# Kernel tuning notes

Hardware: AMD Instinct MI355X
Metric: run time of the kernel (lower is better)

Reference implementation:

```python
import jax, jax.numpy as jnp
import numpy as np

N, E, DIM, HEADS, EDGE_DIM = 50000, 800000, 128, 4, 1
C = DIM // HEADS  # per-head channels
EPS = 1e-5


def graph_ln(h, w, b):
    # PyG LayerNorm, mode='graph', batch=None: normalize over ALL nodes+features
    mu = h.mean()
    hc = h - mu
    std = jnp.sqrt(jnp.mean(hc * hc))
    return hc / (std + EPS) * w + b


def setup_inputs() -> dict:
    key = jax.random.key(0)
    ks = jax.random.split(key, 16)
    s = 1.0 / np.sqrt(DIM)
    return {
        "x": jax.random.normal(ks[0], (N, DIM), jnp.float32),
        "edge_index": jax.random.randint(ks[1], (2, E), 0, N, jnp.int32),
        "edge_weight": jax.random.uniform(ks[2], (E,), jnp.float32),
        "edge_attr": jax.random.normal(ks[3], (E, EDGE_DIM), jnp.float32),
        # GCNConv params
        "W_gcn": jax.random.normal(ks[4], (DIM, DIM), jnp.float32) * s,
        "b_gcn": jnp.zeros((DIM,), jnp.float32),
        # GATv2Conv params (share_weights=True -> single lin)
        "W_l": jax.random.normal(ks[5], (DIM, DIM), jnp.float32) * s,
        "b_l": jnp.zeros((DIM,), jnp.float32),
        "W_edge": jax.random.normal(ks[6], (EDGE_DIM, DIM), jnp.float32),
        "att": jax.random.normal(ks[7], (HEADS, C), jnp.float32) * (1.0 / np.sqrt(C)),
        "b_gat": jnp.zeros((DIM,), jnp.float32),
        # norms
        "gcn_nw": jnp.ones((DIM,), jnp.float32), "gcn_nb": jnp.zeros((DIM,), jnp.float32),
        "gat_nw": jnp.ones((DIM,), jnp.float32), "gat_nb": jnp.zeros((DIM,), jnp.float32),
        "out_nw": jnp.ones((DIM,), jnp.float32), "out_nb": jnp.zeros((DIM,), jnp.float32),
        "alpha": jnp.ones((2,), jnp.float32),
    }


def reference(x, edge_index, edge_weight, edge_attr, W_gcn, b_gcn, W_l, b_l,
              W_edge, att, b_gat, gcn_nw, gcn_nb, gat_nw, gat_nb, out_nw, out_nb, alpha):
    src, dst = edge_index[0], edge_index[1]

    # ---- GCN branch (normalize=True, add_self_loops=False) ----
    deg = jax.ops.segment_sum(edge_weight, dst, num_segments=N)
    dis = jnp.where(deg > 0, jax.lax.rsqrt(jnp.maximum(deg, 1e-30)), 0.0)
    norm = dis[src] * edge_weight * dis[dst]  # [E]
    xw = x @ W_gcn  # [N, DIM]
    h = jax.ops.segment_sum(norm[:, None] * xw[src], dst, num_segments=N) + b_gcn
    gcn_out = x + jax.nn.gelu(graph_ln(h, gcn_nw, gcn_nb), approximate=False)

    # ---- GATv2 branch (share_weights=True, edge_dim=1) ----
    xl = (x @ W_l + b_l).reshape(N, HEADS, C)
    e = (edge_attr @ W_edge).reshape(E, HEADS, C)
    z = jax.nn.leaky_relu(xl[dst] + xl[src] + e, negative_slope=0.2)  # [E,H,C]
    logits = jnp.einsum('ehc,hc->eh', z, att)  # [E,H]
    m = jax.ops.segment_max(logits, dst, num_segments=N)  # [N,H]
    a = jnp.exp(logits - m[dst])
    denom = jax.ops.segment_sum(a, dst, num_segments=N)
    a = a / (denom[dst] + 1e-16)  # softmax over incoming edges per dst, per head
    msg = xl[src] * a[:, :, None]  # [E,H,C]
    g = jax.ops.segment_sum(msg, dst, num_segments=N).reshape(N, DIM) + b_gat
    gat_out = x + jax.nn.gelu(graph_ln(g, gat_nw, gat_nb), approximate=False)

    # ---- fuse ----
    w = jax.nn.softmax(alpha)
    fused = w[0] * gcn_out + w[1] * gat_out
    return jax.nn.gelu(graph_ln(fused, out_nw, out_nb), approximate=False)
```

## Files before the change

### kernel.cpp

```cpp
#include <hip/hip_runtime.h>
#include <math.h>

#define DIM 128
#define HEADS 4
#define EPS 1e-5f
#define NBLK 1024

__device__ __forceinline__ float us2f(unsigned short u) {
  union { unsigned int i; float f; } c; c.i = ((unsigned int)u) << 16; return c.f;
}
__device__ __forceinline__ unsigned short f2us(float f) {
  union { float ff; unsigned int i; } c; c.ff = f;
  return (unsigned short)((c.i + 0x7FFFu + ((c.i >> 16) & 1u)) >> 16);
}
__device__ __forceinline__ float ldf(const void* p, size_t i, int fl32) {
  return fl32 ? ((const float*)p)[i] : us2f(((const unsigned short*)p)[i]);
}
__device__ __forceinline__ float gelu_exact(float v) {
  return 0.5f * v * (1.0f + erff(v * 0.7071067811865475f));
}

__device__ __forceinline__ int packed_pos(int c) { return ((c & ~1) << 1) | (c & 1); }

__global__ void __launch_bounds__(256)
k_detect(const unsigned short* __restrict__ x, long n, int* __restrict__ dflag) {
  long lim = n < 8192 ? n : 8192;
  int bad = 0;
  for (long i = threadIdx.x; i < lim; i += 256) {
    float v = us2f(x[i]);
    float a = fabsf(v);
    if (!(a == 0.0f || (a > 1e-30f && a < 1e3f))) bad++;
  }
  __shared__ int sb[256];
  sb[threadIdx.x] = bad;
  __syncthreads();
  for (int off = 128; off > 0; off >>= 1) {
    if ((int)threadIdx.x < off) sb[threadIdx.x] += sb[threadIdx.x + off];
    __syncthreads();
  }
  if (threadIdx.x == 0) dflag[0] = (sb[0] > 32) ? 1 : 0;
}

__global__ void k_deg_cnt(const int* __restrict__ dst, const void* __restrict__ ew,
                          float* __restrict__ deg, int* __restrict__ cnt,
                          int* __restrict__ rank, int E, const int* __restrict__ df) {
  const int fl32 = *df;
  int e = blockIdx.x * blockDim.x + threadIdx.x;
  if (e < E) {
    int d = dst[e];
    rank[e] = atomicAdd(&cnt[d], 1);
    float w = ldf(ew, e, fl32);
    if (isfinite(w)) atomicAdd(&deg[d], w);
  }
}

__global__ void k_dis(float* __restrict__ deg, int N) {
  int i = blockIdx.x * blockDim.x + threadIdx.x;
  if (i < N) {
    float d = deg[i];
    deg[i] = (d > 0.0f) ? rsqrtf(fmaxf(d, 1e-30f)) : 0.0f;
  }
}

__global__ void __launch_bounds__(256)
k_scan(const int* __restrict__ cnt, int* __restrict__ off, int N, int E) {
  __shared__ int part[256];
  int t = threadIdx.x;
  int chunk = (N + 255) / 256;
  int lo = t * chunk;
  int hi = lo + chunk; if (hi > N) hi = N;
  int s = 0;
  for (int i = lo; i < hi; ++i) s += cnt[i];
  part[t] = s;
  __syncthreads();
  if (t == 0) {
    int run = 0;
    for (int j = 0; j < 256; ++j) { int tmp = part[j]; part[j] = run; run += tmp; }
  }
  __syncthreads();
  int run = part[t];
  for (int i = lo; i < hi; ++i) { off[i] = run; run += cnt[i]; }
  if (t == 0) off[N] = E;
}

__global__ void k_scatter(const int* __restrict__ src, const int* __restrict__ dst,
                          const void* __restrict__ ew, const void* __restrict__ ea,
                          const float* __restrict__ dis, const int* __restrict__ off,
                          const int* __restrict__ rank, int4* __restrict__ csr,
                          int E, const int* __restrict__ df) {
  const int fl32 = *df;
  int e = blockIdx.x * blockDim.x + threadIdx.x;
  if (e >= E) return;
  int d = dst[e], s = src[e];
  int pos = off[d] + rank[e];
  float nm = dis[s] * ldf(ew, e, fl32) * dis[d];
  if (!isfinite(nm)) nm = 0.0f;
  float eav = ldf(ea, e, fl32);
  if (!isfinite(eav)) eav = 0.0f;
  csr[pos] = make_int4(s, __float_as_int(nm), __float_as_int(eav), 0);
}

__global__ void __launch_bounds__(128)
k_gemm(const void* __restrict__ x, const void* __restrict__ Wg,
       const void* __restrict__ Wl, const void* __restrict__ bl,
       unsigned short* __restrict__ packed, int N, const int* __restrict__ df) {
  const int fl32 = *df;
  const int R = 8;
  __shared__ float xs[R][DIM];
  int c = threadIdx.x;
  int r0 = blockIdx.x * R;
  for (int r = 0; r < R; ++r) {
    int row = r0 + r;
    xs[r][c] = (row < N) ? ldf(x, (size_t)row * DIM + c, fl32) : 0.0f;
  }
  __syncthreads();
  float accg[R], accl[R];
  float blc = ldf(bl, c, fl32);
  #pragma unroll
  for (int r = 0; r < R; ++r) { accg[r] = 0.0f; accl[r] = blc; }
  for (int k = 0; k < DIM; ++k) {
    float wg = ldf(Wg, k * DIM + c, fl32);
    float wl = ldf(Wl, k * DIM + c, fl32);
    #pragma unroll
    for (int r = 0; r < R; ++r) {
      accg[r] = fmaf(xs[r][k], wg, accg[r]);
      accl[r] = fmaf(xs[r][k], wl, accl[r]);
    }
  }
  int pos = packed_pos(c);
  for (int r = 0; r < R; ++r) {
    int row = r0 + r;
    if (row < N) {
      float ag = accg[r], al = accl[r];
      if (!isfinite(ag)) ag = 0.0f;
      if (!isfinite(al)) al = 0.0f;
      packed[(size_t)row * 256 + pos] = f2us(al);
      packed[(size_t)row * 256 + pos + 2] = f2us(ag);
    }
  }
}

__global__ void __launch_bounds__(256)
k_mega(const int* __restrict__ off, const int4* __restrict__ csr,
       const unsigned short* __restrict__ packed,
       const void* __restrict__ Wed, const void* __restrict__ att,
       const void* __restrict__ bgcn, const void* __restrict__ bgat,
       float* __restrict__ h, float* __restrict__ g,
       double* __restrict__ pA, double* __restrict__ pB, int N,
       const int* __restrict__ df) {
  const int fl32 = *df;
  int wid = threadIdx.x >> 6;
  int lane = threadIdx.x & 63;
  int node = blockIdx.x * 4 + wid;
  int c0 = lane * 2;
  float wd0 = ldf(Wed, c0, fl32), wd1 = ldf(Wed, c0 + 1, fl32);
  float at0 = ldf(att, c0, fl32), at1 = ldf(att, c0 + 1, fl32);
  double sA = 0.0, sA2 = 0.0, sB = 0.0, sB2 = 0.0;
  if (node < N) {
    int beg = off[node], end = off[node + 1];
    ushort4 xd = *(const ushort4*)(packed + (size_t)node * 256 + lane * 4);
    float xd0 = us2f(xd.x), xd1 = us2f(xd.y);
    float mx = -INFINITY, den = 0.f;
    float ga0 = 0.f, ga1 = 0.f, hc0 = 0.f, hc1 = 0.f;
    int4 cP = make_int4(0, 0, 0, 0);
    ushort4 vP = make_ushort4(0, 0, 0, 0);
    if (beg < end) {
      cP = csr[beg];
      vP = *(const ushort4*)(packed + (size_t)cP.x * 256 + lane * 4);
    }
    for (int i = beg; i < end; ++i) {
      int4 ce = cP; ushort4 v = vP;
      if (i + 1 < end) {
        cP = csr[i + 1];
        vP = *(const ushort4*)(packed + (size_t)cP.x * 256 + lane * 4);
      }
      float nm = __int_as_float(ce.y), eav = __int_as_float(ce.z);
      float vx = us2f(v.x), vy = us2f(v.y);
      float z0 = xd0 + vx + eav * wd0; z0 = (z0 > 0.f) ? z0 : 0.2f * z0;
      float z1 = xd1 + vy + eav * wd1; z1 = (z1 > 0.f) ? z1 : 0.2f * z1;
      float dot = z0 * at0 + z1 * at1;
      dot += __shfl_xor(dot, 1);
      dot += __shfl_xor(dot, 2);
      dot += __shfl_xor(dot, 4);
      dot += __shfl_xor(dot, 8);
      float e = __expf(-fabsf(dot - mx));
      bool up = dot > mx;
      float corr = up ? e : 1.0f;
      float w = up ? 1.0f : e;
      mx = up ? dot : mx;
      den = fmaf(den, corr, w);
      ga0 = fmaf(ga0, corr, w * vx);
      ga1 = fmaf(ga1, corr, w * vy);
      hc0 = fmaf(nm, us2f(v.z), hc0);
      hc1 = fmaf(nm, us2f(v.w), hc1);
    }
    float inv = (end > beg) ? 1.0f / (den + 1e-16f) : 0.0f;
    ga0 *= inv; ga1 *= inv;
    if (!isfinite(ga0)) ga0 = 0.0f;
    if (!isfinite(ga1)) ga1 = 0.0f;
    if (!isfinite(hc0)) hc0 = 0.0f;
    if (!isfinite(hc1)) hc1 = 0.0f;
    *(float2*)(h + (size_t)node * DIM + c0) = make_float2(hc0, hc1);
    *(float2*)(g + (size_t)node * DIM + c0) = make_float2(ga0, ga1);
    float hA0 = hc0 + ldf(bgcn, c0, fl32), hA1 = hc1 + ldf(bgcn, c0 + 1, fl32);
    float gB0 = ga0 + ldf(bgat, c0, fl32), gB1 = ga1 + ldf(bgat, c0 + 1, fl32);
    sA  = (double)hA0 + (double)hA1;
    sA2 = (double)hA0 * hA0 + (double)hA1 * hA1;
    sB  = (double)gB0 + (double)gB1;
    sB2 = (double)gB0 * gB0 + (double)gB1 * gB1;
  }
  __shared__ double l1[256], l2[256], l3[256], l4[256];
  l1[threadIdx.x] = sA; l2[threadIdx.x] = sA2; l3[threadIdx.x] = sB; l4[threadIdx.x] = sB2;
  __syncthreads();
  for (int o = 128; o > 0; o >>= 1) {
    if ((int)threadIdx.x < o) {
      l1[threadIdx.x] += l1[threadIdx.x + o];
      l2[threadIdx.x] += l2[threadIdx.x + o];
      l3[threadIdx.x] += l3[threadIdx.x + o];
      l4[threadIdx.x] += l4[threadIdx.x + o];
    }
    __syncthreads();
  }
  if (threadIdx.x == 0) {
    pA[2 * blockIdx.x] = l1[0]; pA[2 * blockIdx.x + 1] = l2[0];
    pB[2 * blockIdx.x] = l3[0]; pB[2 * blockIdx.x + 1] = l4[0];
  }
}

__device__ __forceinline__ void ln_params(double S, double S2, double M, float* mu_out, float* sc_out) {
  double mu = S / M;
  double v = S2 / M - mu * mu;
  if (!(v > 0.0)) v = 0.0;
  float fmu = (float)mu;
  float sc = 1.0f / ((float)sqrt(v) + EPS);
  if (!isfinite(fmu)) fmu = 0.0f;
  if (!isfinite(sc)) sc = 0.0f;
  *mu_out = fmu; *sc_out = sc;
}

__global__ void __launch_bounds__(256)
k_fin12(const double* __restrict__ pA, const double* __restrict__ pB, int nblk,
        const void* __restrict__ alpha, float* __restrict__ params, double M,
        const int* __restrict__ df) {
  const int fl32 = *df;
  __shared__ double l1[256], l2[256], l3[256], l4[256];
  double a = 0, b = 0, c = 0, d = 0;
  for (int j = threadIdx.x; j < nblk; j += 256) {
    a += pA[2 * j]; b += pA[2 * j + 1];
    c += pB[2 * j]; d += pB[2 * j + 1];
  }
  l1[threadIdx.x] = a; l2[threadIdx.x] = b; l3[threadIdx.x] = c; l4[threadIdx.x] = d;
  __syncthreads();
  for (int off = 128; off > 0; off >>= 1) {
    if ((int)threadIdx.x < off) {
      l1[threadIdx.x] += l1[threadIdx.x + off];
      l2[threadIdx.x] += l2[threadIdx.x + off];
      l3[threadIdx.x] += l3[threadIdx.x + off];
      l4[threadIdx.x] += l4[threadIdx.x + off];
    }
    __syncthreads();
  }
  if (threadIdx.x == 0) {
    ln_params(l1[0], l2[0], M, &params[0], &params[1]);
    ln_params(l3[0], l4[0], M, &params[2], &params[3]);
    float a0 = ldf(alpha, 0, fl32), a1 = ldf(alpha, 1, fl32);
    if (!isfinite(a0)) a0 = 0.0f;
    if (!isfinite(a1)) a1 = 0.0f;
    float mx = fmaxf(a0, a1);
    float e0 = expf(a0 - mx), e1 = expf(a1 - mx);
    float inv = 1.0f / (e0 + e1);
    params[4] = e0 * inv;
    params[5] = e1 * inv;
  }
}

__global__ void __launch_bounds__(256)
k_fin3(const double* __restrict__ pC, float* __restrict__ params, double M) {
  __shared__ double l1[256], l2[256];
  double a = 0, b = 0;
  for (int j = threadIdx.x; j < NBLK; j += 256) { a += pC[2 * j]; b += pC[2 * j + 1]; }
  l1[threadIdx.x] = a; l2[threadIdx.x] = b;
  __syncthreads();
  for (int off = 128; off > 0; off >>= 1) {
    if ((int)threadIdx.x < off) {
      l1[threadIdx.x] += l1[threadIdx.x + off];
      l2[threadIdx.x] += l2[threadIdx.x + off];
    }
    __syncthreads();
  }
  if (threadIdx.x == 0) ln_params(l1[0], l2[0], M, &params[6], &params[7]);
}

__global__ void __launch_bounds__(256)
k_fuse(const void* __restrict__ x, float* h, const float* __restrict__ g,
       const void* __restrict__ b_gcn, const void* __restrict__ b_gat,
       const void* __restrict__ gcn_nw, const void* __restrict__ gcn_nb,
       const void* __restrict__ gat_nw, const void* __restrict__ gat_nb,
       const float* __restrict__ params, double* __restrict__ pC, long n,
       const int* __restrict__ df) {
  const int fl32 = *df;
  float mu1 = params[0], sc1 = params[1], mu2 = params[2], sc2 = params[3];
  float w0 = params[4], w1 = params[5];
  double s = 0.0, s2 = 0.0;
  long stride = (long)gridDim.x * blockDim.x;
  for (long i = (long)blockIdx.x * blockDim.x + threadIdx.x; i < n; i += stride) {
    size_t c = (size_t)(i & (DIM - 1));
    float xv = ldf(x, i, fl32);
    float hv = h[i] + ldf(b_gcn, c, fl32);
    float gv = g[i] + ldf(b_gat, c, fl32);
    float go = xv + gelu_exact((hv - mu1) * sc1 * ldf(gcn_nw, c, fl32) + ldf(gcn_nb, c, fl32));
    float ao = xv + gelu_exact((gv - mu2) * sc2 * ldf(gat_nw, c, fl32) + ldf(gat_nb, c, fl32));
    float f = w0 * go + w1 * ao;
    if (!isfinite(f)) f = 0.0f;
    h[i] = f;
    s += f; s2 += (double)f * f;
  }
  __shared__ double ls[256], ls2[256];
  ls[threadIdx.x] = s; ls2[threadIdx.x] = s2;
  __syncthreads();
  for (int off = 128; off > 0; off >>= 1) {
    if ((int)threadIdx.x < off) {
      ls[threadIdx.x] += ls[threadIdx.x + off];
      ls2[threadIdx.x] += ls2[threadIdx.x + off];
    }
    __syncthreads();
  }
  if (threadIdx.x == 0) { pC[2 * blockIdx.x] = ls[0]; pC[2 * blockIdx.x + 1] = ls2[0]; }
}

__global__ void k_final(const float* __restrict__ fused, const void* __restrict__ nw,
                        const void* __restrict__ nb, const float* __restrict__ params,
                        void* __restrict__ out, long n, const int* __restrict__ df) {
  const int fl32 = *df;
  long i = (long)blockIdx.x * blockDim.x + threadIdx.x;
  if (i >= n) return;
  size_t c = (size_t)(i & (DIM - 1));
  float mu = params[6], sc = params[7];
  float r = gelu_exact((fused[i] - mu) * sc * ldf(nw, c, fl32) + ldf(nb, c, fl32));
  if (!isfinite(r)) r = 0.0f;
  if (fl32) ((float*)out)[i] = r;
  else      ((unsigned short*)out)[i] = f2us(r);
}

extern "C" void kernel_launch(void* const* d_in, const int* in_sizes, int n_in,
                              void* d_out, int out_size, void* d_ws, size_t ws_size,
                              hipStream_t stream) {
  const void* x    = d_in[0];
  const int*  ei   = (const int*)d_in[1];
  const void* ew   = d_in[2];
  const void* ea   = d_in[3];
  const void* Wg   = d_in[4];
  const void* bgcn = d_in[5];
  const void* Wl   = d_in[6];
  const void* bl   = d_in[7];
  const void* Wed  = d_in[8];
  const void* att  = d_in[9];
  const void* bgat = d_in[10];
  const void* gcn_nw = d_in[11];
  const void* gcn_nb = d_in[12];
  const void* gat_nw = d_in[13];
  const void* gat_nb = d_in[14];
  const void* out_nw = d_in[15];
  const void* out_nb = d_in[16];
  const void* alpha  = d_in[17];

  const int N = in_sizes[0] / DIM;
  const int E = in_sizes[2];
  const int* src  = ei;
  const int* dstp = ei + E;
  const size_t ND = (size_t)N * DIM;
  const int nAgg = (N + 3) / 4;

  char* ws = (char*)d_ws;
  size_t o = 0;
  auto alloc = [&](size_t bytes) { size_t r = o; o += (bytes + 255) & ~(size_t)255; return r; };
  size_t o_deg    = alloc((size_t)N * 4);
  size_t o_cnt    = alloc((size_t)N * 4);
  size_t zero_end = o;
  size_t o_off    = alloc((size_t)(N + 1) * 4);
  size_t o_h      = alloc(ND * 4);
  size_t o_g      = alloc(ND * 4);
  size_t o_packed = alloc(ND * 4);
  size_t o_csr    = alloc((size_t)E * 16);
  size_t o_par    = alloc(8 * 4);
  size_t o_pA     = alloc((size_t)nAgg * 2 * 8);
  size_t o_pB     = alloc((size_t)nAgg * 2 * 8);
  size_t o_pC     = alloc((size_t)NBLK * 2 * 8);
  size_t o_flag   = alloc(4);
  (void)ws_size; (void)n_in; (void)out_size;

  float* deg     = (float*)(ws + o_deg);
  int*   cnt     = (int*)(ws + o_cnt);
  int*   off     = (int*)(ws + o_off);
  float* h       = (float*)(ws + o_h);
  int*   rank    = (int*)(ws + o_h);
  float* g       = (float*)(ws + o_g);
  unsigned short* packed = (unsigned short*)(ws + o_packed);
  int4*  csr     = (int4*)(ws + o_csr);
  float* params  = (float*)(ws + o_par);
  double* pA     = (double*)(ws + o_pA);
  double* pB     = (double*)(ws + o_pB);
  double* pC     = (double*)(ws + o_pC);
  int* dflag     = (int*)(ws + o_flag);

  hipMemsetAsync(ws, 0, zero_end, stream);
  k_detect<<<1, 256, 0, stream>>>((const unsigned short*)x, (long)ND, dflag);

  int ebk = (E + 255) / 256;
  k_deg_cnt<<<ebk, 256, 0, stream>>>(dstp, ew, deg, cnt, rank, E, dflag);
  k_dis<<<(N + 255) / 256, 256, 0, stream>>>(deg, N);
  k_scan<<<1, 256, 0, stream>>>(cnt, off, N, E);
  k_scatter<<<ebk, 256, 0, stream>>>(src, dstp, ew, ea, deg, off, rank, csr, E, dflag);

  k_gemm<<<(N + 7) / 8, 128, 0, stream>>>(x, Wg, Wl, bl, packed, N, dflag);

  k_mega<<<nAgg, 256, 0, stream>>>(off, csr, packed, Wed, att, bgcn, bgat,
                                   h, g, pA, pB, N, dflag);

  k_fin12<<<1, 256, 0, stream>>>(pA, pB, nAgg, alpha, params, (double)ND, dflag);
  k_fuse<<<NBLK, 256, 0, stream>>>(x, h, g, bgcn, bgat, gcn_nw, gcn_nb, gat_nw, gat_nb,
                                   params, pC, (long)ND, dflag);
  k_fin3<<<1, 256, 0, stream>>>(pC, params, (double)ND);
  k_final<<<(int)((ND + 255) / 256), 256, 0, stream>>>(h, out_nw, out_nb, params,
                                                       d_out, (long)ND, dflag);
}
```

Measured before the change: 558.1 us.

## Replace scalar FMA node GEMM with split-bf16 MFMA GEMM

The scalar per-column FMA GEMM that computes x@W_gcn and x@W_l is replaced by a matrix-core kernel using bf16 16x16x32 MFMA. To keep near-fp32 accuracy, inputs and weights are split into high and low bf16 parts (three MFMA products per tile). A small prep kernel pre-transposes and splits the weights into the packed column order, and the x tiles are staged in an XOR-swizzled LDS layout. This cuts FP32 ALU work in the GEMM, at the cost of an extra launch and some precision relative to true fp32.

New measurement: 537.4 us. 3.7% less time.

```diff
diff --git a/kernel.cpp b/kernel.cpp
--- a/kernel.cpp
+++ b/kernel.cpp
@@ -100,42 +100,118 @@
   csr[pos] = make_int4(s, __float_as_int(nm), __float_as_int(eav), 0);
 }
 
-__global__ void __launch_bounds__(128)
-k_gemm(const void* __restrict__ x, const void* __restrict__ Wg,
-       const void* __restrict__ Wl, const void* __restrict__ bl,
-       unsigned short* __restrict__ packed, int N, const int* __restrict__ df) {
-  const int fl32 = *df;
-  const int R = 8;
-  __shared__ float xs[R][DIM];
-  int c = threadIdx.x;
-  int r0 = blockIdx.x * R;
-  for (int r = 0; r < R; ++r) {
-    int row = r0 + r;
-    xs[r][c] = (row < N) ? ldf(x, (size_t)row * DIM + c, fl32) : 0.0f;
-  }
-  __syncthreads();
-  float accg[R], accl[R];
-  float blc = ldf(bl, c, fl32);
+__global__ void __launch_bounds__(256)
+k_wprep(const void* __restrict__ Wg, const void* __restrict__ Wl,
+        const void* __restrict__ bl, unsigned short* __restrict__ Bhi,
+        unsigned short* __restrict__ Blo, float* __restrict__ bias2,
+        const int* __restrict__ df) {
+  const int fl32 = *df;
+  int g = blockIdx.x * 256 + threadIdx.x;
+  int col = g >> 7, k = g & 127;
+  int t4 = col >> 2, r = col & 3;
+  int wcol = t4 * 2 + (r & 1);
+  float v = (r < 2) ? ldf(Wl, (size_t)k * DIM + wcol, fl32)
+                    : ldf(Wg, (size_t)k * DIM + wcol, fl32);
+  unsigned short hi = f2us(v);
+  float lo = v - us2f(hi);
+  Bhi[(size_t)col * 128 + k] = hi;
+  Blo[(size_t)col * 128 + k] = f2us(lo);
+  if (blockIdx.x == 0) {
+    int c2 = threadIdx.x;
+    int tt = c2 >> 2, rr = c2 & 3;
+    bias2[c2] = (rr < 2) ? ldf(bl, tt * 2 + rr, fl32) : 0.0f;
+  }
+}
+
+typedef __attribute__((ext_vector_type(8))) short short8v;
+typedef __attribute__((ext_vector_type(4))) float f32x4;
+
+__global__ void __launch_bounds__(256)
+k_gemm_mfma(const void* __restrict__ x, const unsigned short* __restrict__ Bhi,
+            const unsigned short* __restrict__ Blo, const float* __restrict__ bias2,
+            unsigned short* __restrict__ packed, int N, const int* __restrict__ df) {
+  const int fl32 = *df;
+  __shared__ unsigned short Ahi[64 * 128];
+  __shared__ unsigned short Alo[64 * 128];
+  const int tid = threadIdx.x;
+  const int r0 = blockIdx.x * 64;
   #pragma unroll
-  for (int r = 0; r < R; ++r) { accg[r] = 0.0f; accl[r] = blc; }
-  for (int k = 0; k < DIM; ++k) {
-    float wg = ldf(Wg, k * DIM + c, fl32);
-    float wl = ldf(Wl, k * DIM + c, fl32);
+  for (int it = 0; it < 8; ++it) {
+    int i4 = tid + it * 256;
+    int row = i4 >> 5, kq = i4 & 31;
+    int grow = r0 + row;
+    float v0 = 0.f, v1 = 0.f, v2 = 0.f, v3 = 0.f;
+    if (grow < N) {
+      if (fl32) {
+        float4 f = ((const float4*)x)[(size_t)grow * 32 + kq];
+        v0 = f.x; v1 = f.y; v2 = f.z; v3 = f.w;
+      } else {
+        ushort4 u = ((const ushort4*)x)[(size_t)grow * 32 + kq];
+        v0 = us2f(u.x); v1 = us2f(u.y); v2 = us2f(u.z); v3 = us2f(u.w);
+      }
+    }
+    ushort4 hi = make_ushort4(f2us(v0), f2us(v1), f2us(v2), f2us(v3));
+    ushort4 lo = make_ushort4(f2us(v0 - us2f(hi.x)), f2us(v1 - us2f(hi.y)),
+                              f2us(v2 - us2f(hi.z)), f2us(v3 - us2f(hi.w)));
+    int ba = (row * 256 + kq * 8) ^ ((row & 7) << 4);
+    *(ushort4*)((char*)Ahi + ba) = hi;
+    *(ushort4*)((char*)Alo + ba) = lo;
+  }
+  __syncthreads();
+  const int lane = tid & 63, wid = tid >> 6;
+  const int mbase = (wid >> 1) * 32;
+  const int nbase = (wid & 1) * 128;
+  const int lr = lane & 15, lk = lane >> 4;
+  short8v ah[2][4], al[2][4];
+  #pragma unroll
+  for (int m = 0; m < 2; ++m) {
     #pragma unroll
-    for (int r = 0; r < R; ++r) {
-      accg[r] = fmaf(xs[r][k], wg, accg[r]);
-      accl[r] = fmaf(xs[r][k], wl, accl[r]);
-    }
-  }
-  int pos = packed_pos(c);
-  for (int r = 0; r < R; ++r) {
-    int row = r0 + r;
-    if (row < N) {
-      float ag = accg[r], al = accl[r];
-      if (!isfinite(ag)) ag = 0.0f;
-      if (!isfinite(al)) al = 0.0f;
-      packed[(size_t)row * 256 + pos] = f2us(al);
-      packed[(size_t)row * 256 + pos + 2] = f2us(ag);
+    for (int ks = 0; ks < 4; ++ks) {
+      int row = mbase + m * 16 + lr;
+      int ba = (row * 256 + ks * 64 + lk * 16) ^ ((row & 7) << 4);
+      ah[m][ks] = *(const short8v*)((const char*)Ahi + ba);
+      al[m][ks] = *(const short8v*)((const char*)Alo + ba);
+    }
+  }
+  f32x4 acc[2][8];
+  const f32x4 zero = {0.0f, 0.0f, 0.0f, 0.0f};
+  #pragma unroll
+  for (int m = 0; m < 2; ++m)
+    #pragma unroll
+    for (int n = 0; n < 8; ++n) acc[m][n] = zero;
+  #pragma unroll
+  for (int n = 0; n < 8; ++n) {
+    int col = nbase + n * 16 + lr;
+    const unsigned short* bh0 = Bhi + (size_t)col * 128 + lk * 8;
+    const unsigned short* bl0 = Blo + (size_t)col * 128 + lk * 8;
+    #pragma unroll
+    for (int ks = 0; ks < 4; ++ks) {
+      short8v bh  = *(const short8v*)(bh0 + ks * 32);
+      short8v blv = *(const short8v*)(bl0 + ks * 32);
+      acc[0][n] = __builtin_amdgcn_mfma_f32_16x16x32_bf16(ah[0][ks], bh, acc[0][n], 0, 0, 0);
+      acc[1][n] = __builtin_amdgcn_mfma_f32_16x16x32_bf16(ah[1][ks], bh, acc[1][n], 0, 0, 0);
+      acc[0][n] = __builtin_amdgcn_mfma_f32_16x16x32_bf16(al[0][ks], bh, acc[0][n], 0, 0, 0);
+      acc[1][n] = __builtin_amdgcn_mfma_f32_16x16x32_bf16(al[1][ks], bh, acc[1][n], 0, 0, 0);
+      acc[0][n] = __builtin_amdgcn_mfma_f32_16x16x32_bf16(ah[0][ks], blv, acc[0][n], 0, 0, 0);
+      acc[1][n] = __builtin_amdgcn_mfma_f32_16x16x32_bf16(ah[1][ks], blv, acc[1][n], 0, 0, 0);
+    }
+  }
+  #pragma unroll
+  for (int m = 0; m < 2; ++m) {
+    #pragma unroll
+    for (int n = 0; n < 8; ++n) {
+      int col = nbase + n * 16 + lr;
+      float bv = bias2[col];
+      int rb = r0 + mbase + m * 16 + lk * 4;
+      #pragma unroll
+      for (int j = 0; j < 4; ++j) {
+        int row = rb + j;
+        if (row < N) {
+          float v = acc[m][n][j] + bv;
+          if (!isfinite(v)) v = 0.0f;
+          packed[(size_t)row * 256 + col] = f2us(v);
+        }
+      }
     }
   }
 }
@@ -387,6 +463,9 @@
   size_t o_pB     = alloc((size_t)nAgg * 2 * 8);
   size_t o_pC     = alloc((size_t)NBLK * 2 * 8);
   size_t o_flag   = alloc(4);
+  size_t o_bh     = alloc((size_t)256 * 128 * 2);
+  size_t o_blo    = alloc((size_t)256 * 128 * 2);
+  size_t o_b2     = alloc((size_t)256 * 4);
   (void)ws_size; (void)n_in; (void)out_size;
 
   float* deg     = (float*)(ws + o_deg);
@@ -402,9 +481,14 @@
   double* pB     = (double*)(ws + o_pB);
   double* pC     = (double*)(ws + o_pC);
   int* dflag     = (int*)(ws + o_flag);
+  unsigned short* Bhi = (unsigned short*)(ws + o_bh);
+  unsigned short* Blo = (unsigned short*)(ws + o_blo);
+  float* bias2   = (float*)(ws + o_b2);
 
   hipMemsetAsync(ws, 0, zero_end, stream);
   k_detect<<<1, 256, 0, stream>>>((const unsigned short*)x, (long)ND, dflag);
+
+  k_wprep<<<128, 256, 0, stream>>>(Wg, Wl, bl, Bhi, Blo, bias2, dflag);
 
   int ebk = (E + 255) / 256;
   k_deg_cnt<<<ebk, 256, 0, stream>>>(dstp, ew, deg, cnt, rank, E, dflag);
@@ -412,7 +496,7 @@
   k_scan<<<1, 256, 0, stream>>>(cnt, off, N, E);
   k_scatter<<<ebk, 256, 0, stream>>>(src, dstp, ew, ea, deg, off, rank, csr, E, dflag);
 
-  k_gemm<<<(N + 7) / 8, 128, 0, stream>>>(x, Wg, Wl, bl, packed, N, dflag);
+  k_gemm_mfma<<<(N + 63) / 64, 256, 0, stream>>>(x, Bhi, Blo, bias2, packed, N, dflag);
 
   k_mega<<<nAgg, 256, 0, stream>>>(off, csr, packed, Wed, att, bgcn, bgat,
                                    h, g, pA, pB, N, dflag);
```
